# Kernel tuning notes

Hardware: AMD Instinct MI355X
Metric: run time of the kernel (lower is better)

The kernel has to match this reference:

```python
import jax, jax.numpy as jnp
import numpy as np

B, T, D = 1, 4096, 1024
H, DK, DV, L = 16, 64, 64, 32
ROT_SCALE = 1.0  # rotary_pos_scale default


def _rotate_half(x):
    # '... (j d) -> ... j d' with j=2, then cat((-x2, x1))
    x1, x2 = jnp.split(x, 2, axis=-1)
    return jnp.concatenate((-x2, x1), axis=-1)


def _apply_rope(freqs, x, scale):
    # freqs: [T, L] broadcasts over leading dims of x [..., T, L]
    return x * jnp.cos(freqs) * scale + _rotate_half(x) * jnp.sin(freqs) * scale


def setup_inputs() -> dict:
    key = jax.random.key(0)
    ks = jax.random.split(key, 9)
    q = jax.random.normal(ks[0], (B, T, D), jnp.float32)
    k = jax.random.normal(ks[1], (B, T, D), jnp.float32)
    v = jax.random.normal(ks[2], (B, T, D), jnp.float32)
    mask = jnp.tril(jnp.ones((T, T), dtype=bool))  # causal [T, T]
    rotary_freqs = jax.random.normal(ks[3], (T, L), jnp.float32)
    s = 0.02
    w_q = jax.random.normal(ks[4], (H * DK, D), jnp.float32) * s
    w_k = jax.random.normal(ks[5], (H * DK, D), jnp.float32) * s
    w_v = jax.random.normal(ks[6], (H * DV, D), jnp.float32) * s
    w_o = jax.random.normal(ks[7], (D, H * DV), jnp.float32) * s
    return {"q": q, "k": k, "v": v, "mask": mask, "rotary_freqs": rotary_freqs,
            "w_q": w_q, "w_k": w_k, "w_v": w_v, "w_o": w_o}


def reference(q, k, v, mask, rotary_freqs, w_q, w_k, w_v, w_o):
    # project and split heads: '... T (H k) -> ... H T k'
    def heads(x, w, dh):
        y = jnp.einsum('btd,ed->bte', x, w)
        return y.reshape(B, T, H, dh).transpose(0, 2, 1, 3)  # [B,H,T,dh]

    q_i = heads(q, w_q, DK)
    k_i = heads(k, w_k, DK)
    v_i = heads(v, w_v, DV)

    # rotary pos emb on first L dims of q, k AND v (unusual: v too)
    q_scale, k_scale = ROT_SCALE, ROT_SCALE ** (-1.0)

    def rope(x, scale):
        xl, xr = x[..., :L], x[..., L:]
        return jnp.concatenate((_apply_rope(rotary_freqs, xl, scale), xr), axis=-1)

    q_i = rope(q_i, q_scale)
    k_i = rope(k_i, k_scale)
    v_i = rope(v_i, k_scale)

    s_qk = jnp.einsum('bhik,bhjk->bhij', q_i, k_i) / (DK ** 0.5)
    neg = -jnp.finfo(s_qk.dtype).max
    s_qk = jnp.where(mask, s_qk, neg)  # mask broadcasts [T,T] -> [B,H,T,T]
    attn = jax.nn.softmax(s_qk, axis=-1)
    vals = jnp.einsum('bhij,bhjv->bhiv', attn, v_i)
    vals = vals.transpose(0, 2, 1, 3).reshape(B, T, H * DV)  # '... H T v -> ... T (H v)'
    out = jnp.einsum('bte,oe->bto', vals, w_o)
    return out
```

## Files before the change

### kernel.cpp

```cpp
#include <hip/hip_runtime.h>

typedef unsigned short u16;
typedef unsigned int u32;
typedef short bf16x8 __attribute__((ext_vector_type(8)));
typedef float f32x4 __attribute__((ext_vector_type(4)));
typedef unsigned short u16x4 __attribute__((ext_vector_type(4)));
typedef unsigned short u16x8 __attribute__((ext_vector_type(8)));

__device__ __forceinline__ u16 f32_to_bf16(float f) {
    u32 u = __float_as_uint(f);
    u += 0x7FFFu + ((u >> 16) & 1u);
    return (u16)(u >> 16);
}
__device__ __forceinline__ short f32_to_bf16_trunc(float f) {
    return (short)(__float_as_uint(f) >> 16);
}

#if __has_builtin(__builtin_amdgcn_exp2f)
#define EXP2(x) __builtin_amdgcn_exp2f(x)
#else
#define EXP2(x) __expf((x) * 0.69314718056f)
#endif

__device__ __forceinline__ void gl_lds16(const u16* g, u16* l) {
    __builtin_amdgcn_global_load_lds(
        (const __attribute__((address_space(1))) u32*)g,
        (__attribute__((address_space(3))) u32*)l, 16, 0, 0);
}


struct CastArgs {
    const float* src[8];
    u16* dst[8];
    int n4[8];
};

__global__ __launch_bounds__(256) void cast_kernel(CastArgs a) {
    const int y = blockIdx.y;
    const int n4 = a.n4[y];
    if (y == 7) {
        const float* s = a.src[7];
        float* c  = (float*)a.dst[7];
        float* sn = c + 131072;
        for (int i = blockIdx.x * blockDim.x + threadIdx.x; i < n4; i += gridDim.x * blockDim.x) {
            f32x4 v = *(const f32x4*)&s[(size_t)i * 4];
            f32x4 cv, sv;
            #pragma unroll
            for (int j = 0; j < 4; j++) {
                float ss, cc;
                __sincosf(v[j], &ss, &cc);
                sv[j] = ss; cv[j] = cc;
            }
            *(f32x4*)&c[(size_t)i * 4]  = cv;
            *(f32x4*)&sn[(size_t)i * 4] = sv;
        }
        return;
    }
    const float* s = a.src[y];
    u16* d = a.dst[y];
    for (int i = blockIdx.x * blockDim.x + threadIdx.x; i < n4; i += gridDim.x * blockDim.x) {
        f32x4 v = *(const f32x4*)&s[(size_t)i * 4];
        u16x4 o = { f32_to_bf16(v[0]), f32_to_bf16(v[1]), f32_to_bf16(v[2]), f32_to_bf16(v[3]) };
        *(u16x4*)&d[(size_t)i * 4] = o;
    }
}

#define GK 1024
#define GN 1024
#define GM 4096

__global__ __launch_bounds__(256) void gemm_rope(
    const u16* __restrict__ A0, const u16* __restrict__ A1, const u16* __restrict__ A2,
    const u16* __restrict__ W0, const u16* __restrict__ W1, const u16* __restrict__ W2,
    u16* __restrict__ C0, u16* __restrict__ C1, u16* __restrict__ C2,
    const float* __restrict__ freqs, const float* __restrict__ csT)
{
    __shared__ u16 SM[16384];

    const int z = blockIdx.z;
    const u16* A = (z == 0) ? A0 : ((z == 1) ? A1 : A2);
    const u16* W = (z == 0) ? W0 : ((z == 1) ? W1 : W2);
    u16* Cb      = (z == 0) ? C0 : ((z == 1) ? C1 : C2);
    const float ascale = (z == 0) ? 0.18033688f : 1.0f;

    const int tid  = threadIdx.x;
    const int w    = tid >> 6;
    const int lane = tid & 63;
    const int quad = lane >> 4;
    const int l16  = lane & 15;
    const int m0 = blockIdx.x * 128;
    const int n0 = blockIdx.y * 128;
    const int wm = (w >> 1) * 64;
    const int wn = (w & 1) * 64;

    const int sr = tid >> 2;
    const int sc = (((tid & 3) ^ ((tid >> 3) & 3))) * 8;
    const size_t aoff0 = (size_t)(m0 + sr) * GK + sc;
    const size_t aoff1 = aoff0 + (size_t)64 * GK;
    const size_t boff0 = (size_t)(n0 + sr) * GK + sc;
    const size_t boff1 = boff0 + (size_t)64 * GK;

    const int csw = (quad ^ ((l16 >> 1) & 3)) * 8;

    f32x4 acc[4][4];
    for (int i = 0; i < 4; i++)
        for (int j = 0; j < 4; j++) acc[i][j] = 0.f;

    {
        u16* Ab = SM;
        gl_lds16(A + aoff0, &Ab[w * 512]);
        gl_lds16(A + aoff1, &Ab[2048 + w * 512]);
        gl_lds16(W + boff0, &Ab[4096 + w * 512]);
        gl_lds16(W + boff1, &Ab[4096 + 2048 + w * 512]);
    }

    for (int it = 0; it < 32; ++it) {
        __syncthreads();
        if (it < 31) {
            const int k0 = (it + 1) * 32;
            u16* Ab = SM + ((it + 1) & 1) * 8192;
            gl_lds16(A + aoff0 + k0, &Ab[w * 512]);
            gl_lds16(A + aoff1 + k0, &Ab[2048 + w * 512]);
            gl_lds16(W + boff0 + k0, &Ab[4096 + w * 512]);
            gl_lds16(W + boff1 + k0, &Ab[4096 + 2048 + w * 512]);
        }
        const u16* As = SM + (it & 1) * 8192;
        const u16* Bs = As + 4096;

        bf16x8 af[4], bfr[4];
        for (int t = 0; t < 4; t++) {
            af[t]  = *(const bf16x8*)&As[(wm + t * 16 + l16) * 32 + csw];
            bfr[t] = *(const bf16x8*)&Bs[(wn + t * 16 + l16) * 32 + csw];
        }
        for (int mt = 0; mt < 4; mt++)
            for (int nt = 0; nt < 4; nt++)
                acc[mt][nt] = __builtin_amdgcn_mfma_f32_16x16x32_bf16(
                    af[mt], bfr[nt], acc[mt][nt], 0, 0, 0);
    }
    __syncthreads();
    u16* tr = SM + w * 1152;

    const int hh = (n0 + wn) >> 6;
    const size_t tb = (size_t)hh * 262144 + (size_t)((m0 + wm) >> 6) * 4096;
    const float* snT = csT ? (csT + 131072) : (const float*)0;

    if (z != 2) {
        for (int mt = 0; mt < 4; mt++) {
            #pragma unroll
            for (int r = 0; r < 4; r++) {
                int m = m0 + wm + mt * 16 + quad * 4 + r;
                float v0 = acc[mt][0][r];
                float v1 = acc[mt][1][r];
                float s0, c0, s1, c1;
                if (csT) {
                    c0 = csT[m * 32 + l16];      s0 = snT[m * 32 + l16];
                    c1 = csT[m * 32 + 16 + l16]; s1 = snT[m * 32 + 16 + l16];
                } else {
                    __sincosf(freqs[m * 32 + l16], &s0, &c0);
                    __sincosf(freqs[m * 32 + 16 + l16], &s1, &c1);
                }
                int row = quad * 4 + r;
                tr[row * 72 + l16]      = f32_to_bf16((v0 * c0 - v1 * s0) * ascale);
                tr[row * 72 + 16 + l16] = f32_to_bf16((v1 * c1 + v0 * s1) * ascale);
                tr[row * 72 + 32 + l16] = f32_to_bf16(acc[mt][2][r] * ascale);
                tr[row * 72 + 48 + l16] = f32_to_bf16(acc[mt][3][r] * ascale);
            }
            u16x8 va = *(const u16x8*)&tr[l16 * 72 + quad * 16];
            u16x8 vb = *(const u16x8*)&tr[l16 * 72 + quad * 16 + 8];
            if (z == 0) {
                size_t base = (size_t)(m0 + wm + mt * 16 + l16) * GN + n0 + wn + quad * 16;
                *(u16x8*)&Cb[base]     = va;
                *(u16x8*)&Cb[base + 8] = vb;
            } else {
                size_t base = tb + (size_t)(quad >> 1) * 2048
                            + (size_t)(mt * 16 + l16) * 32 + (quad & 1) * 16;
                *(u16x8*)&Cb[base]     = va;
                *(u16x8*)&Cb[base + 8] = vb;
            }
        }
    } else {
        for (int mt = 0; mt < 4; mt++) {
            float o0[4], o1[4];
            for (int r = 0; r < 4; r++) {
                int m = m0 + wm + mt * 16 + quad * 4 + r;
                float v0 = acc[mt][0][r];
                float v1 = acc[mt][1][r];
                float s0, c0, s1, c1;
                if (csT) {
                    c0 = csT[m * 32 + l16];      s0 = snT[m * 32 + l16];
                    c1 = csT[m * 32 + 16 + l16]; s1 = snT[m * 32 + 16 + l16];
                } else {
                    __sincosf(freqs[m * 32 + l16], &s0, &c0);
                    __sincosf(freqs[m * 32 + 16 + l16], &s1, &c1);
                }
                o0[r] = v0 * c0 - v1 * s0;
                o1[r] = v1 * c1 + v0 * s1;
            }
            const int ks = mt >> 1;
            const int sl = 4 * (mt & 1) + 8 * quad;
            const size_t hb = tb + (size_t)ks * 2048 + sl;
            u16x4 u;
            u = { f32_to_bf16(o0[0]), f32_to_bf16(o0[1]), f32_to_bf16(o0[2]), f32_to_bf16(o0[3]) };
            *(u16x4*)&Cb[hb + (size_t)l16 * 32] = u;
            u = { f32_to_bf16(o1[0]), f32_to_bf16(o1[1]), f32_to_bf16(o1[2]), f32_to_bf16(o1[3]) };
            *(u16x4*)&Cb[hb + (size_t)(16 + l16) * 32] = u;
            u = { f32_to_bf16(acc[mt][2][0]), f32_to_bf16(acc[mt][2][1]),
                  f32_to_bf16(acc[mt][2][2]), f32_to_bf16(acc[mt][2][3]) };
            *(u16x4*)&Cb[hb + (size_t)(32 + l16) * 32] = u;
            u = { f32_to_bf16(acc[mt][3][0]), f32_to_bf16(acc[mt][3][1]),
                  f32_to_bf16(acc[mt][3][2]), f32_to_bf16(acc[mt][3][3]) };
            *(u16x4*)&Cb[hb + (size_t)(48 + l16) * 32] = u;
        }
    }
}

__global__ __launch_bounds__(256) void gemm_out(
    const u16* __restrict__ A, const u16* __restrict__ W, float* __restrict__ C)
{
    __shared__ u16 SM[12288];

    const int tid  = threadIdx.x;
    const int w    = tid >> 6;
    const int lane = tid & 63;
    const int quad = lane >> 4;
    const int l16  = lane & 15;
    const int m0 = blockIdx.x * 64;
    const int n0 = blockIdx.y * 128;
    const int wm = (w >> 1) * 32;
    const int wn = (w & 1) * 64;

    const int sr = tid >> 2;
    const int sc = (((tid & 3) ^ ((tid >> 3) & 3))) * 8;
    const size_t aoff  = (size_t)(m0 + sr) * GK + sc;
    const size_t boff0 = (size_t)(n0 + sr) * GK + sc;
    const size_t boff1 = boff0 + (size_t)64 * GK;

    const int csw = (quad ^ ((l16 >> 1) & 3)) * 8;

    f32x4 acc[2][4];
    for (int i = 0; i < 2; i++)
        for (int j = 0; j < 4; j++) acc[i][j] = 0.f;

    {
        u16* Ab = SM;
        gl_lds16(A + aoff,  &Ab[w * 512]);
        gl_lds16(W + boff0, &Ab[2048 + w * 512]);
        gl_lds16(W + boff1, &Ab[2048 + 2048 + w * 512]);
    }

    for (int it = 0; it < 32; ++it) {
        __syncthreads();
        if (it < 31) {
            const int k0 = (it + 1) * 32;
            u16* Ab = SM + ((it + 1) & 1) * 6144;
            gl_lds16(A + aoff + k0,  &Ab[w * 512]);
            gl_lds16(W + boff0 + k0, &Ab[2048 + w * 512]);
            gl_lds16(W + boff1 + k0, &Ab[2048 + 2048 + w * 512]);
        }
        const u16* As = SM + (it & 1) * 6144;
        const u16* Bs = As + 2048;

        bf16x8 af[2], bfr[4];
        for (int t = 0; t < 2; t++)
            af[t] = *(const bf16x8*)&As[(wm + t * 16 + l16) * 32 + csw];
        for (int t = 0; t < 4; t++)
            bfr[t] = *(const bf16x8*)&Bs[(wn + t * 16 + l16) * 32 + csw];
        for (int mt = 0; mt < 2; mt++)
            for (int nt = 0; nt < 4; nt++)
                acc[mt][nt] = __builtin_amdgcn_mfma_f32_16x16x32_bf16(
                    af[mt], bfr[nt], acc[mt][nt], 0, 0, 0);
    }
    __syncthreads();

    float* tr = (float*)SM + w * 1088;
    for (int mt = 0; mt < 2; mt++) {
        #pragma unroll
        for (int nt = 0; nt < 4; nt++)
            #pragma unroll
            for (int r = 0; r < 4; r++)
                tr[(quad * 4 + r) * 68 + nt * 16 + l16] = acc[mt][nt][r];
        size_t base = (size_t)(m0 + wm + mt * 16 + l16) * GN + n0 + wn + quad * 16;
        #pragma unroll
        for (int c = 0; c < 4; c++) {
            f32x4 v = *(const f32x4*)&tr[l16 * 68 + quad * 16 + c * 4];
            *(f32x4*)&C[base + c * 4] = v;
        }
    }
}

__global__ __launch_bounds__(512, 2) void attn_kernel(
    const u16* __restrict__ Qb, const u16* __restrict__ KT,
    const u16* __restrict__ VTg, u16* __restrict__ valsb)
{
    __shared__ __align__(16) u16 KV[2][8192];
    __shared__ __align__(16) float EX[8704];

    const int tid  = threadIdx.x;
    const int w    = tid >> 6;
    const int lane = tid & 63;
    const int quad = lane >> 4;
    const int l16  = lane & 15;
    const int HD = 1024;

    const int id = blockIdx.x;
    const int h  = (id & 7) * 2 + ((id >> 3) & 1);
    const int qb = 63 - (id >> 4);

    const u16* kt = KT  + (size_t)h * 262144;
    const u16* vt = VTg + (size_t)h * 262144;

    const int wq = w >> 1;
    const int wk = w & 1;
    const int wr = w & 3;

    const int dmaoff = (lane >> 2) * 32 + ((lane & 3) ^ ((lane >> 3) & 3)) * 8;
    const int csw = (quad ^ ((l16 >> 1) & 3)) * 8;

    const u16* stsrc = (w < 4) ? kt : vt;
    const int  stdst = (w < 4) ? 0 : 4096;

    bf16x8 ones;
    #pragma unroll
    for (int i = 0; i < 8; i++) ones[i] = (short)0x3F80;
    const f32x4 seed = { -23.0831204f, -23.0831204f, -23.0831204f, -23.0831204f };

    const size_t qrow = (size_t)(qb * 64 + wq * 16 + l16);
    const bf16x8 bq0 = *(const bf16x8*)&Qb[qrow * HD + h * 64 + quad * 8];
    const bf16x8 bq1 = *(const bf16x8*)&Qb[qrow * HD + h * 64 + 32 + quad * 8];
    const int q_local = wq * 16 + l16;

    f32x4 o[4];
    #pragma unroll
    for (int i = 0; i < 4; i++) o[i] = 0.f;
    f32x4 ls_acc = 0.f;

    gl_lds16(stsrc + wr * 512 + dmaoff,        &KV[0][stdst + wr * 512]);
    gl_lds16(stsrc + 2048 + wr * 512 + dmaoff, &KV[0][stdst + 2048 + wr * 512]);

    for (int kb = 0; kb <= qb; kb++) {
        __syncthreads();
        if (kb < qb) {
            const int nb = (kb + 1) & 1;
            const u16* src = stsrc + (size_t)(kb + 1) * 4096;
            gl_lds16(src + wr * 512 + dmaoff,        &KV[nb][stdst + wr * 512]);
            gl_lds16(src + 2048 + wr * 512 + dmaoff, &KV[nb][stdst + 2048 + wr * 512]);
        }
        const u16* Ksb = &KV[kb & 1][0];
        const u16* Vsb = &KV[kb & 1][4096];

        bf16x8 ak[2][2];
        #pragma unroll
        for (int kt2 = 0; kt2 < 2; kt2++) {
            const int krow = wk * 32 + kt2 * 16 + l16;
            ak[kt2][0] = *(const bf16x8*)&Ksb[krow * 32 + csw];
            ak[kt2][1] = *(const bf16x8*)&Ksb[2048 + krow * 32 + csw];
        }

        f32x4 s[2];
        #pragma unroll
        for (int kt2 = 0; kt2 < 2; kt2++) {
            f32x4 z4 = seed;
            z4 = __builtin_amdgcn_mfma_f32_16x16x32_bf16(ak[kt2][0], bq0, z4, 0, 0, 0);
            s[kt2] = __builtin_amdgcn_mfma_f32_16x16x32_bf16(ak[kt2][1], bq1, z4, 0, 0, 0);
        }

        if (kb == qb) {
            #pragma unroll
            for (int kt2 = 0; kt2 < 2; kt2++)
                #pragma unroll
                for (int r = 0; r < 4; r++)
                    if (wk * 32 + kt2 * 16 + quad * 4 + r > q_local) s[kt2][r] = -1e30f;
        }

        bf16x8 av[4];
        #pragma unroll
        for (int nv = 0; nv < 4; nv++)
            av[nv] = *(const bf16x8*)&Vsb[wk * 2048 + (nv * 16 + l16) * 32 + csw];

        #pragma unroll
        for (int kt2 = 0; kt2 < 2; kt2++)
            #pragma unroll
            for (int r = 0; r < 4; r++)
                s[kt2][r] = EXP2(s[kt2][r]);

        bf16x8 bp = { f32_to_bf16_trunc(s[0][0]), f32_to_bf16_trunc(s[0][1]),
                      f32_to_bf16_trunc(s[0][2]), f32_to_bf16_trunc(s[0][3]),
                      f32_to_bf16_trunc(s[1][0]), f32_to_bf16_trunc(s[1][1]),
                      f32_to_bf16_trunc(s[1][2]), f32_to_bf16_trunc(s[1][3]) };

        ls_acc = __builtin_amdgcn_mfma_f32_16x16x32_bf16(ones, bp, ls_acc, 0, 0, 0);

        #pragma unroll
        for (int nv = 0; nv < 4; nv++)
            o[nv] = __builtin_amdgcn_mfma_f32_16x16x32_bf16(av[nv], bp, o[nv], 0, 0, 0);
    }

    const float lsum = ls_acc[0];

    float* my = EX + (w * 64 + lane) * 17;
    #pragma unroll
    for (int nv = 0; nv < 4; nv++) *(f32x4*)&my[nv * 4] = o[nv];
    my[16] = lsum;
    __syncthreads();
    const float* pr = EX + ((w ^ 1) * 64 + lane) * 17;
    f32x4 fin[4];
    #pragma unroll
    for (int nv = 0; nv < 4; nv++) fin[nv] = o[nv] + *(const f32x4*)&pr[nv * 4];
    const float inv = 1.f / (lsum + pr[16]);
    __syncthreads();

    float* myOw = EX + w * 1088;
    #pragma unroll
    for (int nv = 0; nv < 4; nv++)
        #pragma unroll
        for (int r = 0; r < 4; r++)
            myOw[l16 * 68 + nv * 16 + quad * 4 + r] = fin[nv][r] * inv;
    #pragma unroll
    for (int i = 0; i < 2; i++) {
        int row = (wk * 2 + i) * 4 + quad;
        f32x4 vv = *(const f32x4*)&myOw[row * 68 + l16 * 4];
        u16x4 u = { f32_to_bf16(vv[0]), f32_to_bf16(vv[1]), f32_to_bf16(vv[2]), f32_to_bf16(vv[3]) };
        *(u16x4*)&valsb[(size_t)(qb * 64 + wq * 16 + row) * HD + h * 64 + l16 * 4] = u;
    }
}

extern "C" void kernel_launch(void* const* d_in, const int* in_sizes, int n_in,
                              void* d_out, int out_size, void* d_ws, size_t ws_size,
                              hipStream_t stream) {
    const float* q     = (const float*)d_in[0];
    const float* k     = (const float*)d_in[1];
    const float* v     = (const float*)d_in[2];
    const float* freqs = (const float*)d_in[4];
    const float* wq    = (const float*)d_in[5];
    const float* wk    = (const float*)d_in[6];
    const float* wv    = (const float*)d_in[7];
    const float* wo    = (const float*)d_in[8];

    u16* B = (u16*)d_ws;
    u16* qc  = B;
    u16* kc  = B + (size_t)4194304;
    u16* vc  = B + (size_t)8388608;
    u16* wqc = B + (size_t)12582912;
    u16* wkc = B + (size_t)13631488;
    u16* wvc = B + (size_t)14680064;
    u16* woc = B + (size_t)15728640;
    u16* Qb  = B + (size_t)16777216;
    u16* KT  = B + (size_t)20971520;
    u16* VT  = B + (size_t)25165824;
    u16* valsb = qc;

    const size_t tab_off_u16 = 29360128;
    const size_t need_bytes  = 58720256 + 2 * 131072 * sizeof(float);
    float* csT = (ws_size >= need_bytes) ? (float*)(B + tab_off_u16) : (float*)0;

    CastArgs ca;
    ca.src[0] = q;  ca.dst[0] = qc;  ca.n4[0] = 1048576;
    ca.src[1] = k;  ca.dst[1] = kc;  ca.n4[1] = 1048576;
    ca.src[2] = v;  ca.dst[2] = vc;  ca.n4[2] = 1048576;
    ca.src[3] = wq; ca.dst[3] = wqc; ca.n4[3] = 262144;
    ca.src[4] = wk; ca.dst[4] = wkc; ca.n4[4] = 262144;
    ca.src[5] = wv; ca.dst[5] = wvc; ca.n4[5] = 262144;
    ca.src[6] = wo; ca.dst[6] = woc; ca.n4[6] = 262144;
    ca.src[7] = freqs; ca.dst[7] = (u16*)csT; ca.n4[7] = csT ? 32768 : 0;
    cast_kernel<<<dim3(1024, 8), 256, 0, stream>>>(ca);

    gemm_rope<<<dim3(32, 8, 3), 256, 0, stream>>>(
        qc, kc, vc, wqc, wkc, wvc, Qb, KT, VT, freqs, csT);

    attn_kernel<<<dim3(1024), 512, 0, stream>>>(Qb, KT, VT, valsb);

    gemm_out<<<dim3(64, 8), 256, 0, stream>>>(valsb, woc, (float*)d_out);
}
```

Baseline: 258.7 us.

## Restructure attention to 4 waves each owning full key blocks, 128-key stages

The attention kernel drops from 8 waves splitting each 64-key block across two waves to 4 waves that each process all 64 keys for their 16 query rows. This removes the cross-wave LDS reduction of partial outputs and row sums along with its barriers, so results are normalized and stored straight from registers. K/V staging now loads two 64-key blocks (128 keys) per double-buffered stage, halving the number of barriers. In exchange there are fewer waves per block, more registers per wave, and twice the LDS per buffer, which may lower latency hiding.

```diff
diff --git a/kernel.cpp b/kernel.cpp
--- a/kernel.cpp
+++ b/kernel.cpp
@@ -288,12 +288,11 @@
     }
 }
 
-__global__ __launch_bounds__(512, 2) void attn_kernel(
+__global__ __launch_bounds__(256, 2) void attn_kernel(
     const u16* __restrict__ Qb, const u16* __restrict__ KT,
     const u16* __restrict__ VTg, u16* __restrict__ valsb)
 {
-    __shared__ __align__(16) u16 KV[2][8192];
-    __shared__ __align__(16) float EX[8704];
+    __shared__ __align__(16) u16 KV[2][16384];
 
     const int tid  = threadIdx.x;
     const int w    = tid >> 6;
@@ -309,118 +308,111 @@
     const u16* kt = KT  + (size_t)h * 262144;
     const u16* vt = VTg + (size_t)h * 262144;
 
-    const int wq = w >> 1;
-    const int wk = w & 1;
-    const int wr = w & 3;
-
     const int dmaoff = (lane >> 2) * 32 + ((lane & 3) ^ ((lane >> 3) & 3)) * 8;
     const int csw = (quad ^ ((l16 >> 1) & 3)) * 8;
-
-    const u16* stsrc = (w < 4) ? kt : vt;
-    const int  stdst = (w < 4) ? 0 : 4096;
 
     bf16x8 ones;
     #pragma unroll
     for (int i = 0; i < 8; i++) ones[i] = (short)0x3F80;
     const f32x4 seed = { -23.0831204f, -23.0831204f, -23.0831204f, -23.0831204f };
 
-    const size_t qrow = (size_t)(qb * 64 + wq * 16 + l16);
+    const size_t qrow = (size_t)(qb * 64 + w * 16 + l16);
     const bf16x8 bq0 = *(const bf16x8*)&Qb[qrow * HD + h * 64 + quad * 8];
     const bf16x8 bq1 = *(const bf16x8*)&Qb[qrow * HD + h * 64 + 32 + quad * 8];
-    const int q_local = wq * 16 + l16;
+    const int q_local = w * 16 + l16;
 
     f32x4 o[4];
     #pragma unroll
     for (int i = 0; i < 4; i++) o[i] = 0.f;
     f32x4 ls_acc = 0.f;
 
-    gl_lds16(stsrc + wr * 512 + dmaoff,        &KV[0][stdst + wr * 512]);
-    gl_lds16(stsrc + 2048 + wr * 512 + dmaoff, &KV[0][stdst + 2048 + wr * 512]);
-
-    for (int kb = 0; kb <= qb; kb++) {
+    const int T = (qb >> 1) + 1;
+
+    #pragma unroll
+    for (int i = 0; i < 4; i++) {
+        gl_lds16(kt + i * 2048 + w * 512 + dmaoff, &KV[0][i * 2048 + w * 512]);
+        gl_lds16(vt + i * 2048 + w * 512 + dmaoff, &KV[0][8192 + i * 2048 + w * 512]);
+    }
+
+    for (int t = 0; t < T; ++t) {
         __syncthreads();
-        if (kb < qb) {
-            const int nb = (kb + 1) & 1;
-            const u16* src = stsrc + (size_t)(kb + 1) * 4096;
-            gl_lds16(src + wr * 512 + dmaoff,        &KV[nb][stdst + wr * 512]);
-            gl_lds16(src + 2048 + wr * 512 + dmaoff, &KV[nb][stdst + 2048 + wr * 512]);
-        }
-        const u16* Ksb = &KV[kb & 1][0];
-        const u16* Vsb = &KV[kb & 1][4096];
-
-        bf16x8 ak[2][2];
+        if (t < T - 1) {
+            const int nb = (t + 1) & 1;
+            const u16* ksrc = kt + (size_t)(t + 1) * 8192;
+            const u16* vsrc = vt + (size_t)(t + 1) * 8192;
+            #pragma unroll
+            for (int i = 0; i < 4; i++) {
+                gl_lds16(ksrc + i * 2048 + w * 512 + dmaoff, &KV[nb][i * 2048 + w * 512]);
+                gl_lds16(vsrc + i * 2048 + w * 512 + dmaoff, &KV[nb][8192 + i * 2048 + w * 512]);
+            }
+        }
+        const u16* base = &KV[t & 1][0];
+
         #pragma unroll
-        for (int kt2 = 0; kt2 < 2; kt2++) {
-            const int krow = wk * 32 + kt2 * 16 + l16;
-            ak[kt2][0] = *(const bf16x8*)&Ksb[krow * 32 + csw];
-            ak[kt2][1] = *(const bf16x8*)&Ksb[2048 + krow * 32 + csw];
-        }
-
-        f32x4 s[2];
-        #pragma unroll
-        for (int kt2 = 0; kt2 < 2; kt2++) {
-            f32x4 z4 = seed;
-            z4 = __builtin_amdgcn_mfma_f32_16x16x32_bf16(ak[kt2][0], bq0, z4, 0, 0, 0);
-            s[kt2] = __builtin_amdgcn_mfma_f32_16x16x32_bf16(ak[kt2][1], bq1, z4, 0, 0, 0);
-        }
-
-        if (kb == qb) {
-            #pragma unroll
-            for (int kt2 = 0; kt2 < 2; kt2++)
+        for (int sub = 0; sub < 2; ++sub) {
+            const int kb = 2 * t + sub;
+            if (kb > qb) break;
+            const u16* Ksb = base + sub * 4096;
+            const u16* Vsb = base + 8192 + sub * 4096;
+
+            f32x4 s[4];
+            #pragma unroll
+            for (int nt2 = 0; nt2 < 4; nt2++) {
+                bf16x8 ak0 = *(const bf16x8*)&Ksb[(nt2 * 16 + l16) * 32 + csw];
+                bf16x8 ak1 = *(const bf16x8*)&Ksb[2048 + (nt2 * 16 + l16) * 32 + csw];
+                f32x4 z4 = seed;
+                z4 = __builtin_amdgcn_mfma_f32_16x16x32_bf16(ak0, bq0, z4, 0, 0, 0);
+                s[nt2] = __builtin_amdgcn_mfma_f32_16x16x32_bf16(ak1, bq1, z4, 0, 0, 0);
+            }
+
+            if (kb == qb) {
+                #pragma unroll
+                for (int nt2 = 0; nt2 < 4; nt2++)
+                    #pragma unroll
+                    for (int r = 0; r < 4; r++)
+                        if (nt2 * 16 + quad * 4 + r > q_local) s[nt2][r] = -1e30f;
+            }
+
+            bf16x8 av[8];
+            #pragma unroll
+            for (int nv = 0; nv < 4; nv++) {
+                av[nv * 2]     = *(const bf16x8*)&Vsb[(nv * 16 + l16) * 32 + csw];
+                av[nv * 2 + 1] = *(const bf16x8*)&Vsb[2048 + (nv * 16 + l16) * 32 + csw];
+            }
+
+            #pragma unroll
+            for (int nt2 = 0; nt2 < 4; nt2++)
                 #pragma unroll
                 for (int r = 0; r < 4; r++)
-                    if (wk * 32 + kt2 * 16 + quad * 4 + r > q_local) s[kt2][r] = -1e30f;
-        }
-
-        bf16x8 av[4];
-        #pragma unroll
-        for (int nv = 0; nv < 4; nv++)
-            av[nv] = *(const bf16x8*)&Vsb[wk * 2048 + (nv * 16 + l16) * 32 + csw];
-
-        #pragma unroll
-        for (int kt2 = 0; kt2 < 2; kt2++)
-            #pragma unroll
-            for (int r = 0; r < 4; r++)
-                s[kt2][r] = EXP2(s[kt2][r]);
-
-        bf16x8 bp = { f32_to_bf16_trunc(s[0][0]), f32_to_bf16_trunc(s[0][1]),
-                      f32_to_bf16_trunc(s[0][2]), f32_to_bf16_trunc(s[0][3]),
-                      f32_to_bf16_trunc(s[1][0]), f32_to_bf16_trunc(s[1][1]),
-                      f32_to_bf16_trunc(s[1][2]), f32_to_bf16_trunc(s[1][3]) };
-
-        ls_acc = __builtin_amdgcn_mfma_f32_16x16x32_bf16(ones, bp, ls_acc, 0, 0, 0);
-
-        #pragma unroll
-        for (int nv = 0; nv < 4; nv++)
-            o[nv] = __builtin_amdgcn_mfma_f32_16x16x32_bf16(av[nv], bp, o[nv], 0, 0, 0);
-    }
-
-    const float lsum = ls_acc[0];
-
-    float* my = EX + (w * 64 + lane) * 17;
+                    s[nt2][r] = EXP2(s[nt2][r]);
+
+            bf16x8 bp0 = { f32_to_bf16_trunc(s[0][0]), f32_to_bf16_trunc(s[0][1]),
+                           f32_to_bf16_trunc(s[0][2]), f32_to_bf16_trunc(s[0][3]),
+                           f32_to_bf16_trunc(s[1][0]), f32_to_bf16_trunc(s[1][1]),
+                           f32_to_bf16_trunc(s[1][2]), f32_to_bf16_trunc(s[1][3]) };
+            bf16x8 bp1 = { f32_to_bf16_trunc(s[2][0]), f32_to_bf16_trunc(s[2][1]),
+                           f32_to_bf16_trunc(s[2][2]), f32_to_bf16_trunc(s[2][3]),
+                           f32_to_bf16_trunc(s[3][0]), f32_to_bf16_trunc(s[3][1]),
+                           f32_to_bf16_trunc(s[3][2]), f32_to_bf16_trunc(s[3][3]) };
+
+            ls_acc = __builtin_amdgcn_mfma_f32_16x16x32_bf16(ones, bp0, ls_acc, 0, 0, 0);
+            ls_acc = __builtin_amdgcn_mfma_f32_16x16x32_bf16(ones, bp1, ls_acc, 0, 0, 0);
+
+            #pragma unroll
+            for (int nv = 0; nv < 4; nv++) {
+                o[nv] = __builtin_amdgcn_mfma_f32_16x16x32_bf16(av[nv * 2], bp0, o[nv], 0, 0, 0);
+                o[nv] = __builtin_amdgcn_mfma_f32_16x16x32_bf16(av[nv * 2 + 1], bp1, o[nv], 0, 0, 0);
+            }
+        }
+    }
+
+    const float inv = 1.f / ls_acc[0];
+    const size_t obase = (size_t)(qb * 64 + w * 16 + l16) * HD + h * 64;
     #pragma unroll
-    for (int nv = 0; nv < 4; nv++) *(f32x4*)&my[nv * 4] = o[nv];
-    my[16] = lsum;
-    __syncthreads();
-    const float* pr = EX + ((w ^ 1) * 64 + lane) * 17;
-    f32x4 fin[4];
-    #pragma unroll
-    for (int nv = 0; nv < 4; nv++) fin[nv] = o[nv] + *(const f32x4*)&pr[nv * 4];
-    const float inv = 1.f / (lsum + pr[16]);
-    __syncthreads();
-
-    float* myOw = EX + w * 1088;
-    #pragma unroll
-    for (int nv = 0; nv < 4; nv++)
-        #pragma unroll
-        for (int r = 0; r < 4; r++)
-            myOw[l16 * 68 + nv * 16 + quad * 4 + r] = fin[nv][r] * inv;
-    #pragma unroll
-    for (int i = 0; i < 2; i++) {
-        int row = (wk * 2 + i) * 4 + quad;
-        f32x4 vv = *(const f32x4*)&myOw[row * 68 + l16 * 4];
-        u16x4 u = { f32_to_bf16(vv[0]), f32_to_bf16(vv[1]), f32_to_bf16(vv[2]), f32_to_bf16(vv[3]) };
-        *(u16x4*)&valsb[(size_t)(qb * 64 + wq * 16 + row) * HD + h * 64 + l16 * 4] = u;
+    for (int nv = 0; nv < 4; nv++) {
+        u16x4 st = { f32_to_bf16(o[nv][0] * inv), f32_to_bf16(o[nv][1] * inv),
+                     f32_to_bf16(o[nv][2] * inv), f32_to_bf16(o[nv][3] * inv) };
+        *(u16x4*)&valsb[obase + nv * 16 + quad * 4] = st;
     }
 }
 
@@ -467,7 +459,7 @@
     gemm_rope<<<dim3(32, 8, 3), 256, 0, stream>>>(
         qc, kc, vc, wqc, wkc, wvc, Qb, KT, VT, freqs, csT);
 
-    attn_kernel<<<dim3(1024), 512, 0, stream>>>(Qb, KT, VT, valsb);
+    attn_kernel<<<dim3(1024), 256, 0, stream>>>(Qb, KT, VT, valsb);
 
     gemm_out<<<dim3(64, 8), 256, 0, stream>>>(valsb, woc, (float*)d_out);
 }
```

After: 261.6 us. About the same (+1.1%).
